# Optimization experiments

Measured on AMD Instinct MI355X. Metric: run time of the kernel, lower is better.

## Reference

```python
import jax, jax.numpy as jnp
import numpy as np

FILTER_LENGTH = 1024
HOP_LENGTH = 512
CUTOFF = FILTER_LENGTH // 2 + 1  # 513
PAD_AMOUNT = FILTER_LENGTH // 2  # 512


def _make_forward_basis():
    # DFT matrix rows (real stacked over imag, up to Nyquist), windowed by periodic Hann.
    fb = np.fft.fft(np.eye(FILTER_LENGTH))
    fb = np.vstack([np.real(fb[:CUTOFF, :]), np.imag(fb[:CUTOFF, :])])  # [1026, 1024]
    n = np.arange(FILTER_LENGTH)
    # scipy get_window('hann', N, fftbins=True) == periodic Hann
    win = 0.5 * (1.0 - np.cos(2.0 * np.pi * n / FILTER_LENGTH))
    basis = (fb * win[None, :]).astype(np.float32)
    return basis[:, None, :]  # [out_ch=1026, in_ch=1, k=1024]


def setup_inputs() -> dict:
    key = jax.random.key(0)
    audio = jax.random.normal(key, (15360000,), dtype=jnp.float32)
    forward_basis = jnp.asarray(_make_forward_basis())
    return {"audio": audio, "forward_basis": forward_basis}


def reference(audio, forward_basis):
    # [L] -> [1, 1, L + 2*pad] with reflect padding
    x = jnp.pad(audio, (PAD_AMOUNT, PAD_AMOUNT), mode="reflect")[None, None, :]
    # Strided conv1d == windowed DFT per frame; output [1, 1026, n_frames]
    ft = jax.lax.conv_general_dilated(
        x,
        forward_basis,
        window_strides=(HOP_LENGTH,),
        padding="VALID",
        dimension_numbers=("NCH", "OIH", "NCH"),
    )
    real = ft[:, :CUTOFF, :]
    imag = ft[:, CUTOFF:, :]
    return real * real + imag * imag  # power spectrum [1, 513, n_frames]
```

## Files before the change

kernel.cpp:

```cpp
#include <hip/hip_runtime.h>

#define L_AUDIO 15360000
#define PADLEN  15361024
#define FRAMES  30001
#define NBAS    (1026*1024)

#define BM   256
#define BK   64
#define NKT  16
#define NGEMM 472
#define NWG   504

typedef __attribute__((ext_vector_type(8))) short short8;
typedef __attribute__((ext_vector_type(4))) float f32x4;

__device__ __forceinline__ unsigned short f2bf(float f) {
    unsigned int u = __float_as_uint(f);
    u += 0x7fffu + ((u >> 16) & 1u);
    return (unsigned short)(u >> 16);
}

__global__ __launch_bounds__(256) void prep_pad_k(const float* __restrict__ a,
                                                  unsigned short* __restrict__ pad) {
    long i = (long)blockIdx.x * blockDim.x + threadIdx.x;
    long p0 = i * 4;
    if (p0 >= 512 && p0 + 4 <= 512 + L_AUDIO) {
        const float4 v = *reinterpret_cast<const float4*>(a + (p0 - 512));
        ushort4 o;
        o.x = f2bf(v.x); o.y = f2bf(v.y); o.z = f2bf(v.z); o.w = f2bf(v.w);
        *reinterpret_cast<ushort4*>(pad + p0) = o;
    } else {
        for (int j = 0; j < 4; ++j) {
            long p = p0 + j;
            long src = p - 512;
            if (p < 512) src = 512 - p;
            else if (src >= L_AUDIO) src = 2L*L_AUDIO - 2 - src;
            pad[p] = f2bf(a[src]);
        }
    }
}

__global__ __launch_bounds__(256) void prep_bas_k(const float* __restrict__ b,
                                                  unsigned short* __restrict__ o) {
    long i = (long)blockIdx.x * blockDim.x + threadIdx.x;
    const float4 v = *reinterpret_cast<const float4*>(b + i * 4);
    ushort4 u;
    u.x = f2bf(v.x); u.y = f2bf(v.y); u.z = f2bf(v.z); u.w = f2bf(v.w);
    *reinterpret_cast<ushort4*>(o + i * 4) = u;
}

__global__ __launch_bounds__(512, 2) void stft_gemm(const unsigned short* __restrict__ pad,
                                                    const unsigned short* __restrict__ bas,
                                                    const float* __restrict__ bas32,
                                                    float* __restrict__ out) {
    __shared__ unsigned short lsA[2][BM * BK];
    __shared__ unsigned short lsB[2][BM * BK];

    const int tid = threadIdx.x;

    const int bid = blockIdx.x;
    const int wg  = (bid & 7) * 63 + (bid >> 3);

    if (wg >= NGEMM) {
        const int k    = wg - NGEMM;
        const int base = k * 938;
        const int lim  = (base + 938 < FRAMES) ? base + 938 : FRAMES;
        const float* br = bas32 + (long)512  * 1024;
        const float* bi = bas32 + (long)1025 * 1024;
        float* o512 = out + (long)512 * FRAMES;
        #pragma unroll
        for (int rep = 0; rep < 2; ++rep) {
            const int f = base + rep * 512 + tid;
            if (f < lim) {
                const unsigned short* ap = pad + (long)f * 512;
                float re = 0.f, im = 0.f;
                for (int n = 0; n < 1024; n += 8) {
                    short8 a8 = *reinterpret_cast<const short8*>(ap + n);
                    #pragma unroll
                    for (int u = 0; u < 8; ++u) {
                        float av = __uint_as_float(((unsigned)(unsigned short)a8[u]) << 16);
                        re = fmaf(av, br[n + u], re);
                        im = fmaf(av, bi[n + u], im);
                    }
                }
                o512[f] = re * re + im * im;
            }
        }
        return;
    }

    const int w    = tid >> 6;
    const int lane = tid & 63;
    const int l15  = lane & 15;
    const int lk   = lane >> 4;
    const int wm   = w >> 2;
    const int wn   = w & 3;

    const int  fb = wg >> 2;
    const int  cb = wg & 3;
    const long t0 = (long)fb * BM;
    const int  c0 = cb * 128;

    const int sc = (tid & 7) ^ ((tid >> 3) & 7);
    const unsigned short* aS[4];
    #pragma unroll
    for (int j = 0; j < 4; ++j) {
        long tf = t0 + j * 64 + (tid >> 3);
        if (tf > FRAMES - 1) tf = FRAMES - 1;
        aS[j] = pad + tf * 512 + sc * 8;
    }
    const int ch0 = c0 + ((tid >> 8) << 4) + ((tid >> 3) & 15);
    const long brow0 = ch0 + (((tid >> 7) & 1) ? 513 : 0);
    const unsigned short* bS0 = bas + brow0 * 1024 + sc * 8;

    f32x4 acc[8][4];
    #pragma unroll
    for (int a = 0; a < 8; ++a)
        #pragma unroll
        for (int b = 0; b < 4; ++b)
            acc[a][b] = (f32x4){0.f, 0.f, 0.f, 0.f};

    const int wmBase = wm * 128;
    const int wnBase = wn * 64;

#define GLD(dst, src) __builtin_amdgcn_global_load_lds( \
        (const __attribute__((address_space(1))) unsigned int*)(src), \
        (__attribute__((address_space(3))) unsigned int*)(dst), 16, 0, 0)

#define LDSREAD(basePtr, r, S) \
    (*reinterpret_cast<const short8*>(reinterpret_cast<const char*>(basePtr) \
        + (r) * 128 + ((((S) * 4 + lk) ^ ((r) & 7)) << 4)))

#define PHASE_RA(MQ, S) do { _Pragma("unroll") \
    for (int j = 0; j < 4; ++j) { \
        const int r = wmBase + ((MQ) * 4 + j) * 16 + l15; \
        af[j] = LDSREAD(curA, r, S); } } while (0)

#define PHASE_RB(S) do { _Pragma("unroll") \
    for (int b = 0; b < 4; ++b) { \
        const int r = wnBase + b * 16 + l15; \
        bf[b] = LDSREAD(curB, r, S); } } while (0)

#define PHASE_MFMA(MQ) do { \
    __builtin_amdgcn_s_setprio(1); \
    _Pragma("unroll") for (int b_ = 0; b_ < 4; ++b_) \
      _Pragma("unroll") for (int m_ = 0; m_ < 4; ++m_) \
        acc[(MQ)*4+m_][b_] = __builtin_amdgcn_mfma_f32_16x16x32_bf16( \
            af[m_], bf[b_], acc[(MQ)*4+m_][b_], 0, 0, 0); \
    __builtin_amdgcn_s_setprio(0); } while (0)

    #pragma unroll
    for (int j = 0; j < 4; ++j) {
        GLD(&lsA[0][j * 4096 + tid * 8], aS[j]);
        GLD(&lsB[0][j * 4096 + tid * 8], bS0 + j * 32768);
    }

    short8 af[4], bf[4];

    for (int t = 0; t < NKT; ++t) {
        const int p = t & 1;
        const unsigned short* curA = lsA[p];
        const unsigned short* curB = lsB[p];
        unsigned short* nxtA = lsA[p ^ 1];
        unsigned short* nxtB = lsB[p ^ 1];
        const bool more = (t + 1 < NKT);
        const int ko = (t + 1) * BK;

        if (more) { GLD(nxtA + 0 * 4096 + tid * 8, aS[0] + ko);
                    GLD(nxtA + 1 * 4096 + tid * 8, aS[1] + ko); }
        if (more) asm volatile("s_waitcnt vmcnt(2)" ::: "memory");
        else      asm volatile("s_waitcnt vmcnt(0)" ::: "memory");
        __builtin_amdgcn_s_barrier();

        PHASE_RA(0, 0); PHASE_RB(0);
        if (more) { GLD(nxtA + 2 * 4096 + tid * 8, aS[2] + ko);
                    GLD(nxtA + 3 * 4096 + tid * 8, aS[3] + ko); }
        __builtin_amdgcn_s_barrier();
        PHASE_MFMA(0);
        __builtin_amdgcn_s_barrier();

        PHASE_RA(1, 0);
        if (more) { GLD(nxtB + 0 * 4096 + tid * 8, bS0 + 0 * 32768 + ko);
                    GLD(nxtB + 1 * 4096 + tid * 8, bS0 + 1 * 32768 + ko); }
        __builtin_amdgcn_s_barrier();
        PHASE_MFMA(1);
        __builtin_amdgcn_s_barrier();

        PHASE_RA(0, 1); PHASE_RB(1);
        if (more) { GLD(nxtB + 2 * 4096 + tid * 8, bS0 + 2 * 32768 + ko);
                    GLD(nxtB + 3 * 4096 + tid * 8, bS0 + 3 * 32768 + ko); }
        __builtin_amdgcn_s_barrier();
        PHASE_MFMA(0);
        __builtin_amdgcn_s_barrier();

        PHASE_RA(1, 1);
        __builtin_amdgcn_s_barrier();
        PHASE_MFMA(1);
        __builtin_amdgcn_s_barrier();
    }

    const int tb = (int)t0 + wmBase;
    #pragma unroll
    for (int a = 0; a < 8; ++a) {
        #pragma unroll
        for (int q = 0; q < 2; ++q) {
            const int ch = c0 + wn * 32 + q * 16 + l15;
            const long ob = (long)ch * FRAMES;
            const int tv = tb + a * 16 + lk * 4;
            const f32x4 re = acc[a][q * 2];
            const f32x4 im = acc[a][q * 2 + 1];
            if (tv + 3 < FRAMES) {
                #pragma unroll
                for (int r = 0; r < 4; ++r)
                    out[ob + tv + r] = re[r] * re[r] + im[r] * im[r];
            } else {
                #pragma unroll
                for (int r = 0; r < 4; ++r)
                    if (tv + r < FRAMES)
                        out[ob + tv + r] = re[r] * re[r] + im[r] * im[r];
            }
        }
    }
}

extern "C" void kernel_launch(void* const* d_in, const int* in_sizes, int n_in,
                              void* d_out, int out_size, void* d_ws, size_t ws_size,
                              hipStream_t stream) {
    const float* audio = (const float*)d_in[0];
    const float* basis = (const float*)d_in[1];
    float* out = (float*)d_out;

    unsigned short* pad = (unsigned short*)d_ws;
    unsigned short* bas = pad + PADLEN;

    prep_pad_k<<<PADLEN / 4 / 256, 256, 0, stream>>>(audio, pad);
    prep_bas_k<<<NBAS / 4 / 256, 256, 0, stream>>>(basis, bas);

    stft_gemm<<<NWG, 512, 0, stream>>>(pad, bas, basis, out);
}
```

Baseline: 122.2 us.

## Rebalance Nyquist-channel side work across waves with shared half-frame dot products

Changes the grid to 512 workgroups, with a per-XCD split of 59 GEMM workgroups and 5 workgroups that compute the Nyquist channel (512). The Nyquist work is now done one frame per wavefront with a cross-lane shuffle reduction. Each half-frame dot product is computed once and reused for two adjacent frames, since consecutive frames overlap by half. This cuts redundant loads and the serial per-thread loops, but it relies on the Nyquist imaginary part being zero and on basis symmetry between frame halves. The change could also shift the load balance of the tail workgroups.

```diff
diff --git a/kernel.cpp b/kernel.cpp
--- a/kernel.cpp
+++ b/kernel.cpp
@@ -8,8 +8,7 @@
 #define BM   256
 #define BK   64
 #define NKT  16
-#define NGEMM 472
-#define NWG   504
+#define NWG  512
 
 typedef __attribute__((ext_vector_type(8))) short short8;
 typedef __attribute__((ext_vector_type(4))) float f32x4;
@@ -56,41 +55,53 @@
     __shared__ unsigned short lsA[2][BM * BK];
     __shared__ unsigned short lsB[2][BM * BK];
 
-    const int tid = threadIdx.x;
-
-    const int bid = blockIdx.x;
-    const int wg  = (bid & 7) * 63 + (bid >> 3);
-
-    if (wg >= NGEMM) {
-        const int k    = wg - NGEMM;
-        const int base = k * 938;
-        const int lim  = (base + 938 < FRAMES) ? base + 938 : FRAMES;
-        const float* br = bas32 + (long)512  * 1024;
-        const float* bi = bas32 + (long)1025 * 1024;
-        float* o512 = out + (long)512 * FRAMES;
-        #pragma unroll
-        for (int rep = 0; rep < 2; ++rep) {
-            const int f = base + rep * 512 + tid;
-            if (f < lim) {
-                const unsigned short* ap = pad + (long)f * 512;
-                float re = 0.f, im = 0.f;
-                for (int n = 0; n < 1024; n += 8) {
-                    short8 a8 = *reinterpret_cast<const short8*>(ap + n);
-                    #pragma unroll
-                    for (int u = 0; u < 8; ++u) {
-                        float av = __uint_as_float(((unsigned)(unsigned short)a8[u]) << 16);
-                        re = fmaf(av, br[n + u], re);
-                        im = fmaf(av, bi[n + u], im);
-                    }
+    const int tid  = threadIdx.x;
+    const int bid  = blockIdx.x;
+    const int xcd  = bid & 7;
+    const int lid  = bid >> 3;
+
+    const int w    = tid >> 6;
+    const int lane = tid & 63;
+
+    if (lid >= 59) {
+        const int k  = xcd * 5 + (lid - 59);
+        const int F0 = k * 751;
+        const int F1 = (F0 + 751 < FRAMES) ? F0 + 751 : FRAMES;
+        int a = F0 + w * 94;
+        int b = a + 94; if (b > F1) b = F1;
+        if (a < b) {
+            const float* brA = bas32 + (long)512 * 1024 + lane * 8;
+            float bA[8], bB[8];
+            #pragma unroll
+            for (int j = 0; j < 8; ++j) { bA[j] = brA[j]; bB[j] = brA[512 + j]; }
+            float* o512 = out + (long)512 * FRAMES;
+            float prev_p0 = 0.f;
+            for (int u = a; u <= b; ++u) {
+                short8 a8 = *reinterpret_cast<const short8*>(pad + (long)u * 512 + lane * 8);
+                float p0 = 0.f, p1 = 0.f;
+                #pragma unroll
+                for (int j = 0; j < 8; ++j) {
+                    float av = __uint_as_float(((unsigned)(unsigned short)a8[j]) << 16);
+                    p0 = fmaf(av, bA[j], p0);
+                    p1 = fmaf(av, bB[j], p1);
                 }
-                o512[f] = re * re + im * im;
+                #pragma unroll
+                for (int off = 32; off; off >>= 1) {
+                    p0 += __shfl_xor(p0, off, 64);
+                    p1 += __shfl_xor(p1, off, 64);
+                }
+                if (u > a && lane == 0) {
+                    const float v = prev_p0 + p1;
+                    o512[u - 1] = v * v;
+                }
+                prev_p0 = p0;
             }
         }
         return;
     }
 
-    const int w    = tid >> 6;
-    const int lane = tid & 63;
+    const int wg = xcd * 59 + lid;
+
     const int l15  = lane & 15;
     const int lk   = lane >> 4;
     const int wm   = w >> 2;
```

New measurement: 115.0 us. 5.9% less time.
